# Optimization experiments

Hardware: AMD Instinct MI355X
Metric: run time of the kernel (lower is better)

## Reference

```python
import jax, jax.numpy as jnp
import numpy as np

B, S, D, E, H, K = 2, 2048, 1024, 8, 4096, 2


def setup_inputs() -> dict:
    key = jax.random.key(0)
    ks = jax.random.split(key, 7)
    sd = 1.0 / np.sqrt(D)
    sh = 1.0 / np.sqrt(H)
    return {
        "x": jax.random.normal(ks[0], (B, S, D), dtype=jnp.float32),
        "router_w": jax.random.uniform(ks[1], (D, E), jnp.float32, -sd, sd),
        "router_b": jnp.zeros((E,), jnp.float32),
        "w1": jax.random.uniform(ks[2], (E, D, H), jnp.float32, -sd, sd),
        "b1": jnp.zeros((E, H), jnp.float32),
        "w2": jax.random.uniform(ks[3], (E, H, D), jnp.float32, -sh, sh),
        "b2": jnp.zeros((E, D), jnp.float32),
    }


def reference(x, router_w, router_b, w1, b1, w2, b2):
    # Router: softmax over experts, then top-k and renormalize
    router_logits = jnp.einsum("bsd,de->bse", x, router_w) + router_b
    router_probs = jax.nn.softmax(router_logits, axis=-1)
    top_k_probs, top_k_indices = jax.lax.top_k(router_probs, K)  # [B,S,K]
    top_k_probs = top_k_probs / jnp.sum(top_k_probs, axis=-1, keepdims=True)

    # Dense all-expert FFN (Block assumed: Linear -> GELU -> Linear)
    h = jax.nn.gelu(jnp.einsum("bsd,edh->bseh", x, w1) + b1)  # [B,S,E,H]
    expert_outputs = jnp.einsum("bseh,ehd->bsed", h, w2) + b2  # [B,S,E,D]

    # Gather top-k experts per token and combine with renormalized probs
    idx = top_k_indices[..., None]  # [B,S,K,1]
    selected = jnp.take_along_axis(expert_outputs, idx, axis=2)  # [B,S,K,D]
    return jnp.sum(selected * top_k_probs[..., None], axis=2)  # [B,S,D]
```

## Files before the change

### kernel.cpp

```cpp
#include <hip/hip_runtime.h>
#include <hip/hip_bf16.h>

#define TOK   4096
#define DDIM  1024
#define NEXP  8
#define HDIM  4096
#define KSEL  2
#define NPAIR (TOK * KSEL)
#define NSPLIT 4

typedef __attribute__((ext_vector_type(8))) _Float16 f16x8;
typedef __attribute__((ext_vector_type(4))) _Float16 f16x4;
typedef __attribute__((ext_vector_type(4))) float    f32x4;

__device__ __forceinline__ void gload16(const void* g, void* l) {
  __builtin_amdgcn_global_load_lds((const __attribute__((address_space(1))) void*)g,
                                   (__attribute__((address_space(3))) void*)l, 16, 0, 0);
}

__device__ __forceinline__ float gelu_tanh(float u) {
  float inner = 0.7978845608028654f * (u + 0.044715f * u * u * u);
  float t2 = __expf(2.f * inner);
  return u - u / (t2 + 1.f);
}

__global__ __launch_bounds__(256) void k_router(const float* __restrict__ x,
    const float* __restrict__ rw, const float* __restrict__ rb,
    int* __restrict__ tidx, float* __restrict__ tw,
    _Float16* __restrict__ xb) {
  const int t    = blockIdx.x * 4 + (threadIdx.x >> 6);
  const int lane = threadIdx.x & 63;
  const float* xr = x + (size_t)t * DDIM;
  _Float16*   xbr = xb + (size_t)t * DDIM;
  float acc[NEXP];
#pragma unroll
  for (int e = 0; e < NEXP; ++e) acc[e] = 0.f;
  for (int d0 = lane * 4; d0 < DDIM; d0 += 256) {
    const float4 xv = *(const float4*)(xr + d0);
    f16x4 hx;
    hx[0] = (_Float16)xv.x; hx[1] = (_Float16)xv.y;
    hx[2] = (_Float16)xv.z; hx[3] = (_Float16)xv.w;
    *(f16x4*)(xbr + d0) = hx;
#pragma unroll
    for (int i = 0; i < 4; ++i) {
      const float xs = (&xv.x)[i];
      const float4 r0 = *(const float4*)(rw + (size_t)(d0 + i) * NEXP);
      const float4 r1 = *(const float4*)(rw + (size_t)(d0 + i) * NEXP + 4);
      acc[0] += xs * r0.x; acc[1] += xs * r0.y; acc[2] += xs * r0.z; acc[3] += xs * r0.w;
      acc[4] += xs * r1.x; acc[5] += xs * r1.y; acc[6] += xs * r1.z; acc[7] += xs * r1.w;
    }
  }
#pragma unroll
  for (int e = 0; e < NEXP; ++e) {
    float v = acc[e];
#pragma unroll
    for (int s = 32; s; s >>= 1) v += __shfl_xor(v, s, 64);
    acc[e] = v;
  }
  if (lane == 0) {
    float lg[NEXP];
#pragma unroll
    for (int e = 0; e < NEXP; ++e) lg[e] = acc[e] + rb[e];
    int i0 = 0;
#pragma unroll
    for (int e = 1; e < NEXP; ++e) if (lg[e] > lg[i0]) i0 = e;
    int i1 = -1; float best = -3.4e38f;
#pragma unroll
    for (int e = 0; e < NEXP; ++e) {
      if (e == i0) continue;
      if (lg[e] > best) { best = lg[e]; i1 = e; }
    }
    float w0 = 1.f / (1.f + expf(lg[i1] - lg[i0]));
    tidx[t * 2]     = i0;  tidx[t * 2 + 1] = i1;
    tw[t * 2]       = w0;  tw[t * 2 + 1]   = 1.f - w0;
  }
}

__global__ __launch_bounds__(1024) void k_scan(const int* __restrict__ tidx,
                       const float* __restrict__ tw,
                       int* __restrict__ offs,
                       int* __restrict__ row_token, float* __restrict__ row_w,
                       int* __restrict__ inv) {
  __shared__ int hist[NEXP];
  __shared__ int soff[NEXP + 1];
  __shared__ int scur[NEXP];
  if (threadIdx.x < NEXP) hist[threadIdx.x] = 0;
  __syncthreads();
  const int lane = threadIdx.x & 63;
  int e_loc[NPAIR / 1024];
#pragma unroll
  for (int it = 0; it < NPAIR / 1024; ++it) {
    const int p = it * 1024 + threadIdx.x;
    const int e = tidx[p];
    e_loc[it] = e;
#pragma unroll
    for (int ee = 0; ee < NEXP; ++ee) {
      unsigned long long m = __ballot(e == ee);
      if (m && lane == 0) atomicAdd(&hist[ee], __popcll(m));
    }
  }
  __syncthreads();
  if (threadIdx.x == 0) {
    int run = 0;
    for (int e = 0; e < NEXP; ++e) { soff[e] = run; scur[e] = run; run += hist[e]; }
    soff[NEXP] = run;
    for (int e = 0; e <= NEXP; ++e) offs[e] = soff[e];
  }
  __syncthreads();
#pragma unroll
  for (int it = 0; it < NPAIR / 1024; ++it) {
    const int p = it * 1024 + threadIdx.x;
    const int e = e_loc[it];
    int pos = 0;
#pragma unroll
    for (int ee = 0; ee < NEXP; ++ee) {
      unsigned long long m = __ballot(e == ee);
      if (!m) continue;
      int base = 0;
      if (lane == 0) base = atomicAdd(&scur[ee], __popcll(m));
      base = __shfl(base, 0, 64);
      if (e == ee) pos = base + __popcll(m & ((1ull << lane) - 1ull));
    }
    row_token[pos] = p >> 1;
    row_w[pos]     = tw[p];
    inv[p]         = pos;
  }
}

__global__ __launch_bounds__(256) void k_transpose2(const float* __restrict__ w1,
    const float* __restrict__ w2, _Float16* __restrict__ w1t, _Float16* __restrict__ w2t) {
  __shared__ _Float16 tile[64][72];
  const int zz = blockIdx.y;
  const float* ip; _Float16* op; int Rr, Cc, i0, j0;
  if (zz < NEXP) {
    ip = w1 + (size_t)zz * DDIM * HDIM;  op = w1t + (size_t)zz * DDIM * HDIM;
    Rr = DDIM; Cc = HDIM;
    i0 = (blockIdx.x >> 6) * 64; j0 = (blockIdx.x & 63) * 64;
  } else {
    ip = w2 + (size_t)(zz - NEXP) * HDIM * DDIM;  op = w2t + (size_t)(zz - NEXP) * HDIM * DDIM;
    Rr = HDIM; Cc = DDIM;
    i0 = (blockIdx.x >> 4) * 64; j0 = (blockIdx.x & 15) * 64;
  }
  const int tx = threadIdx.x & 15, ty = threadIdx.x >> 4;
#pragma unroll
  for (int rr = 0; rr < 4; ++rr) {
    int r = ty + rr * 16;
    float4 v = *(const float4*)(ip + (size_t)(i0 + r) * Cc + j0 + tx * 4);
    tile[r][tx * 4 + 0] = (_Float16)v.x;
    tile[r][tx * 4 + 1] = (_Float16)v.y;
    tile[r][tx * 4 + 2] = (_Float16)v.z;
    tile[r][tx * 4 + 3] = (_Float16)v.w;
  }
  __syncthreads();
#pragma unroll
  for (int cc = 0; cc < 4; ++cc) {
    int c = ty + cc * 16;
    f16x4 o;
#pragma unroll
    for (int k = 0; k < 4; ++k) o[k] = tile[tx * 4 + k][c];
    *(f16x4*)(op + (size_t)(j0 + c) * Rr + i0 + tx * 4) = o;
  }
}

#define BM 128
#define BN 128
#define BKK 32


__global__ __launch_bounds__(256) void k_gemm1(
    const _Float16* __restrict__ xb,
    const _Float16* __restrict__ w1t,
    const float* __restrict__ b1,
    const int* __restrict__ offs,
    const int* __restrict__ row_token,
    _Float16* __restrict__ hbuf) {
  const int e    = blockIdx.z;
  const int off0 = offs[e];
  const int ne   = offs[e + 1] - off0;
  const int m0   = blockIdx.y * BM;
  if (m0 >= ne) return;
  const int n0   = blockIdx.x * BN;
  const int mrem = ne - m0;

  __shared__ __align__(16) char smem[32768];

  const int tid = threadIdx.x;
  const int wv = tid >> 6, lane = tid & 63;
  const int l15 = lane & 15;
  const int wr = wv >> 1, wc = wv & 1;

  const int rA0 = (wv * 2 + 0) * 16 + (lane >> 2);
  const int rA1 = (wv * 2 + 1) * 16 + (lane >> 2);
  const char* a_c = (const char*)xb;
  const char* b_c = (const char*)(w1t + (size_t)e * HDIM * DDIM);
  const int rc0 = (rA0 < mrem) ? rA0 : (mrem - 1);
  const int rc1 = (rA1 < mrem) ? rA1 : (mrem - 1);
  const char* ap0 = a_c + (size_t)row_token[off0 + m0 + rc0] * (DDIM * 2)
                        + (((lane & 3) ^ ((rA0 >> 1) & 3)) << 4);
  const char* ap1 = a_c + (size_t)row_token[off0 + m0 + rc1] * (DDIM * 2)
                        + (((lane & 3) ^ ((rA1 >> 1) & 3)) << 4);
  const char* bp0 = b_c + (size_t)(n0 + rA0) * (DDIM * 2)
                        + (((lane & 3) ^ ((rA0 >> 1) & 3)) << 4);
  const char* bp1 = b_c + (size_t)(n0 + rA1) * (DDIM * 2)
                        + (((lane & 3) ^ ((rA1 >> 1) & 3)) << 4);
  char* ldsA0 = smem + (wv * 2 + 0) * 1024;
  char* ldsA1 = smem + (wv * 2 + 1) * 1024;
  char* ldsB0 = smem + 16384 + (wv * 2 + 0) * 1024;
  char* ldsB1 = smem + 16384 + (wv * 2 + 1) * 1024;

  const unsigned foff = (unsigned)(((lane >> 4) ^ ((l15 >> 1) & 3)) << 4);

  f32x4 acc[4][4] = {};
  const int NT = DDIM / BKK;

  gload16(ap0, ldsA0); gload16(ap1, ldsA1);
  gload16(bp0, ldsB0); gload16(bp1, ldsB1);
  asm volatile("s_waitcnt vmcnt(0)" ::: "memory");
  __builtin_amdgcn_s_barrier();

#pragma unroll 2
  for (int ks = 0; ks < NT; ++ks) {
    const int cur = ks & 1;
    if (ks + 1 < NT) {
      const int nb = (cur ^ 1) * 8192;
      const size_t kb = (size_t)(ks + 1) * 64;
      gload16(ap0 + kb, ldsA0 + nb); gload16(ap1 + kb, ldsA1 + nb);
      gload16(bp0 + kb, ldsB0 + nb); gload16(bp1 + kb, ldsB1 + nb);
    }
    const char* Ab = smem + cur * 8192;
    const char* Bb = smem + 16384 + cur * 8192;
    f16x8 af[4], bfr[4];
#pragma unroll
    for (int m = 0; m < 4; ++m)
      af[m] = *(const f16x8*)(Ab + (wr * 64 + m * 16 + l15) * 64 + foff);
#pragma unroll
    for (int n = 0; n < 4; ++n)
      bfr[n] = *(const f16x8*)(Bb + (wc * 64 + n * 16 + l15) * 64 + foff);
#pragma unroll
    for (int m = 0; m < 4; ++m)
#pragma unroll
      for (int n = 0; n < 4; ++n)
        acc[m][n] = __builtin_amdgcn_mfma_f32_16x16x32_f16(af[m], bfr[n], acc[m][n], 0, 0, 0);
    __builtin_amdgcn_sched_barrier(0);
    asm volatile("s_waitcnt vmcnt(0)" ::: "memory");
    __builtin_amdgcn_s_barrier();
  }

  float bias[4];
#pragma unroll
  for (int n = 0; n < 4; ++n)
    bias[n] = b1[(size_t)e * HDIM + n0 + wc * 64 + n * 16 + l15];
#pragma unroll
  for (int m = 0; m < 4; ++m) {
#pragma unroll
    for (int j = 0; j < 4; ++j) {
      int row = wr * 64 + m * 16 + (lane >> 4) * 4 + j;
#pragma unroll
      for (int n = 0; n < 4; ++n) {
        int col = wc * 64 + n * 16 + l15;
        *(_Float16*)(smem + (row << 8) + (((col << 1) ^ ((row & 15) << 4)))) =
            (_Float16)gelu_tanh(acc[m][n][j] + bias[n]);
      }
    }
  }
  __syncthreads();
  {
    const int srow = tid >> 1, half = tid & 1;
    if (srow < mrem) {
      _Float16* hr = hbuf + (size_t)(off0 + m0 + srow) * HDIM + n0 + half * 64;
#pragma unroll
      for (int i = 0; i < 8; ++i) {
        f16x8 v = *(const f16x8*)(smem + (srow << 8) + (((half * 128 + i * 16) ^ ((srow & 15) << 4))));
        *(f16x8*)(hr + i * 8) = v;
      }
    }
  }
}

template <bool YB>
__global__ __launch_bounds__(256) void k_gemm2(
    const _Float16* __restrict__ hbuf,
    const _Float16* __restrict__ w2t,
    const float* __restrict__ b2,
    const int* __restrict__ offs,
    const int* __restrict__ row_token,
    const float* __restrict__ row_w,
    _Float16* __restrict__ yb,
    float* __restrict__ out) {
  const int zz = blockIdx.z;
  const int e  = zz >> 2;
  const int kh = zz & 3;
  const int off0 = offs[e];
  const int ne   = offs[e + 1] - off0;
  const int m0   = blockIdx.y * BM;
  if (m0 >= ne) return;
  const int n0   = blockIdx.x * BN;
  const int mrem = ne - m0;

  __shared__ __align__(16) char smem[32768];

  const int tid = threadIdx.x;
  const int wv = tid >> 6, lane = tid & 63;
  const int l15 = lane & 15;
  const int wr = wv >> 1, wc = wv & 1;

  const int rA0 = (wv * 2 + 0) * 16 + (lane >> 2);
  const int rA1 = (wv * 2 + 1) * 16 + (lane >> 2);
  const char* a_c = (const char*)hbuf;
  const char* b_c = (const char*)(w2t + (size_t)e * DDIM * HDIM);
  const int rc0 = (rA0 < mrem) ? rA0 : (mrem - 1);
  const int rc1 = (rA1 < mrem) ? rA1 : (mrem - 1);
  const size_t khb = (size_t)kh * ((HDIM / NSPLIT) * 2);
  const char* ap0 = a_c + (size_t)(off0 + m0 + rc0) * (HDIM * 2) + khb
                        + (((lane & 3) ^ ((rA0 >> 1) & 3)) << 4);
  const char* ap1 = a_c + (size_t)(off0 + m0 + rc1) * (HDIM * 2) + khb
                        + (((lane & 3) ^ ((rA1 >> 1) & 3)) << 4);
  const char* bp0 = b_c + (size_t)(n0 + rA0) * (HDIM * 2) + khb
                        + (((lane & 3) ^ ((rA0 >> 1) & 3)) << 4);
  const char* bp1 = b_c + (size_t)(n0 + rA1) * (HDIM * 2) + khb
                        + (((lane & 3) ^ ((rA1 >> 1) & 3)) << 4);
  char* ldsA0 = smem + (wv * 2 + 0) * 1024;
  char* ldsA1 = smem + (wv * 2 + 1) * 1024;
  char* ldsB0 = smem + 16384 + (wv * 2 + 0) * 1024;
  char* ldsB1 = smem + 16384 + (wv * 2 + 1) * 1024;

  const unsigned foff = (unsigned)(((lane >> 4) ^ ((l15 >> 1) & 3)) << 4);

  f32x4 acc[4][4] = {};
  const int NT = (HDIM / NSPLIT) / BKK;

  gload16(ap0, ldsA0); gload16(ap1, ldsA1);
  gload16(bp0, ldsB0); gload16(bp1, ldsB1);
  asm volatile("s_waitcnt vmcnt(0)" ::: "memory");
  __builtin_amdgcn_s_barrier();

#pragma unroll 2
  for (int ks = 0; ks < NT; ++ks) {
    const int cur = ks & 1;
    if (ks + 1 < NT) {
      const int nb = (cur ^ 1) * 8192;
      const size_t kb = (size_t)(ks + 1) * 64;
      gload16(ap0 + kb, ldsA0 + nb); gload16(ap1 + kb, ldsA1 + nb);
      gload16(bp0 + kb, ldsB0 + nb); gload16(bp1 + kb, ldsB1 + nb);
    }
    const char* Ab = smem + cur * 8192;
    const char* Bb = smem + 16384 + cur * 8192;
    f16x8 af[4], bfr[4];
#pragma unroll
    for (int m = 0; m < 4; ++m)
      af[m] = *(const f16x8*)(Ab + (wr * 64 + m * 16 + l15) * 64 + foff);
#pragma unroll
    for (int n = 0; n < 4; ++n)
      bfr[n] = *(const f16x8*)(Bb + (wc * 64 + n * 16 + l15) * 64 + foff);
#pragma unroll
    for (int m = 0; m < 4; ++m)
#pragma unroll
      for (int n = 0; n < 4; ++n)
        acc[m][n] = __builtin_amdgcn_mfma_f32_16x16x32_f16(af[m], bfr[n], acc[m][n], 0, 0, 0);
    __builtin_amdgcn_sched_barrier(0);
    asm volatile("s_waitcnt vmcnt(0)" ::: "memory");
    __builtin_amdgcn_s_barrier();
  }

  if (YB) {
    _Float16* ypart = yb + (size_t)kh * NPAIR * DDIM;
#pragma unroll
    for (int m = 0; m < 4; ++m) {
#pragma unroll
      for (int j = 0; j < 4; ++j) {
        int row = wr * 64 + m * 16 + (lane >> 4) * 4 + j;
#pragma unroll
        for (int n = 0; n < 4; ++n) {
          int col = wc * 64 + n * 16 + l15;
          *(_Float16*)(smem + (row << 8) + (((col << 1) ^ ((row & 15) << 4)))) =
              (_Float16)acc[m][n][j];
        }
      }
    }
    __syncthreads();
    const int srow = tid >> 1, half = tid & 1;
    if (srow < mrem) {
      _Float16* yr = ypart + (size_t)(off0 + m0 + srow) * DDIM + n0 + half * 64;
#pragma unroll
      for (int i = 0; i < 8; ++i) {
        f16x8 v = *(const f16x8*)(smem + (srow << 8) + (((half * 128 + i * 16) ^ ((srow & 15) << 4))));
        *(f16x8*)(yr + i * 8) = v;
      }
    }
  } else {
    float bias[4];
#pragma unroll
    for (int n = 0; n < 4; ++n)
      bias[n] = (kh == 0) ? b2[(size_t)e * DDIM + n0 + wc * 64 + n * 16 + l15] : 0.f;
#pragma unroll
    for (int m = 0; m < 4; ++m) {
#pragma unroll
      for (int j = 0; j < 4; ++j) {
        int row = wr * 64 + m * 16 + (lane >> 4) * 4 + j;
        if (row < mrem) {
          int g = off0 + m0 + row;
          float wgt = row_w[g];
          float* op = out + (size_t)row_token[g] * DDIM + n0 + wc * 64 + l15;
#pragma unroll
          for (int n = 0; n < 4; ++n)
            atomicAdd(op + n * 16, wgt * (acc[m][n][j] + bias[n]));
        }
      }
    }
  }
}

__global__ __launch_bounds__(256) void k_combine(const _Float16* __restrict__ yb,
    const int* __restrict__ inv, const int* __restrict__ tidx,
    const float* __restrict__ tw, const float* __restrict__ b2,
    float* __restrict__ out) {
  const int t  = blockIdx.x * 2 + (threadIdx.x >> 7);
  const int c8 = (threadIdx.x & 127) * 8;
  const int g0 = inv[2 * t],  g1 = inv[2 * t + 1];
  const int e0 = tidx[2 * t], e1 = tidx[2 * t + 1];
  const float w0 = tw[2 * t], w1 = tw[2 * t + 1];
  float s0[8] = {0,0,0,0,0,0,0,0}, s1[8] = {0,0,0,0,0,0,0,0};
#pragma unroll
  for (int p = 0; p < NSPLIT; ++p) {
    const _Float16* yp = yb + (size_t)p * NPAIR * DDIM;
    f16x8 a = *(const f16x8*)(yp + (size_t)g0 * DDIM + c8);
    f16x8 b = *(const f16x8*)(yp + (size_t)g1 * DDIM + c8);
#pragma unroll
    for (int i = 0; i < 8; ++i) { s0[i] += (float)a[i]; s1[i] += (float)b[i]; }
  }
  float o[8];
#pragma unroll
  for (int i = 0; i < 8; ++i) {
    float bA = b2[(size_t)e0 * DDIM + c8 + i];
    float bB = b2[(size_t)e1 * DDIM + c8 + i];
    o[i] = w0 * (s0[i] + bA) + w1 * (s1[i] + bB);
  }
  float* op = out + (size_t)t * DDIM + c8;
  *(float4*)op       = make_float4(o[0], o[1], o[2], o[3]);
  *(float4*)(op + 4) = make_float4(o[4], o[5], o[6], o[7]);
}

extern "C" void kernel_launch(void* const* d_in, const int* in_sizes, int n_in,
                              void* d_out, int out_size, void* d_ws, size_t ws_size,
                              hipStream_t stream) {
  const float* x  = (const float*)d_in[0];
  const float* rw = (const float*)d_in[1];
  const float* rb = (const float*)d_in[2];
  const float* w1 = (const float*)d_in[3];
  const float* b1 = (const float*)d_in[4];
  const float* w2 = (const float*)d_in[5];
  const float* b2 = (const float*)d_in[6];
  float* out = (float*)d_out;
  char* ws = (char*)d_ws;

  int*      tidx    = (int*)(ws + 0);
  float*    tw      = (float*)(ws + 32768);
  int*      offs    = (int*)(ws + 65792);
  int*      row_tok = (int*)(ws + 66048);
  float*    row_w   = (float*)(ws + 98816);
  int*      inv     = (int*)(ws + 131584);
  _Float16* xb      = (_Float16*)(ws + 164352);
  _Float16* wtA     = (_Float16*)(ws + 8552960);
  _Float16* wtB     = (_Float16*)(ws + 75661824);
  _Float16* hb      = (_Float16*)(ws + 142770688);
  _Float16* yb      = wtA;
  const bool big = ws_size >= 209879552ULL;

  if (!big) hipMemsetAsync(out, 0, (size_t)TOK * DDIM * sizeof(float), stream);

  k_router<<<dim3(TOK / 4), 256, 0, stream>>>(x, rw, rb, tidx, tw, xb);
  k_scan<<<dim3(1), 1024, 0, stream>>>(tidx, tw, offs, row_tok, row_w, inv);
  k_transpose2<<<dim3(1024, 2 * NEXP), 256, 0, stream>>>(w1, w2, wtA, wtB);
  k_gemm1<<<dim3(HDIM / BN, TOK / BM, NEXP), 256, 0, stream>>>(xb, wtA, b1, offs, row_tok, hb);
  if (big) {
    k_gemm2<true><<<dim3(DDIM / BN, TOK / BM, NEXP * NSPLIT), 256, 0, stream>>>(
        hb, wtB, b2, offs, row_tok, row_w, yb, out);
    k_combine<<<dim3(TOK / 2), 256, 0, stream>>>(yb, inv, tidx, tw, b2, out);
  } else {
    k_gemm2<false><<<dim3(DDIM / BN, TOK / BM, NEXP * NSPLIT), 256, 0, stream>>>(
        hb, wtB, b2, offs, row_tok, row_w, yb, out);
  }
}
```

Measured before the change: 385.5 us.

## Use compact tile list for grouped GEMMs and overlap prefetch with barrier

The scan kernel now builds a compact list of (expert, m-tile) pairs, and both grouped GEMMs launch a flat 1D grid over that list instead of a sparse 3D grid where most blocks exit early. The K-loop now waits with vmcnt(4) so the next tile's loads stay in flight while the current one is consumed, rather than fully draining every iteration. The atomic-output fallback path is removed, so the fp16 split-K buffer and combine kernel are always used. MAXT=72 caps the tile count, which assumes expert loads never need more than 72 tiles.

Measured after the change: 356.0 us. 7.7% less time.

```diff
diff --git a/kernel.cpp b/kernel.cpp
--- a/kernel.cpp
+++ b/kernel.cpp
@@ -8,6 +8,7 @@
 #define KSEL  2
 #define NPAIR (TOK * KSEL)
 #define NSPLIT 4
+#define MAXT  72
 
 typedef __attribute__((ext_vector_type(8))) _Float16 f16x8;
 typedef __attribute__((ext_vector_type(4))) _Float16 f16x4;
@@ -80,7 +81,8 @@
                        const float* __restrict__ tw,
                        int* __restrict__ offs,
                        int* __restrict__ row_token, float* __restrict__ row_w,
-                       int* __restrict__ inv) {
+                       int* __restrict__ inv,
+                       int* __restrict__ tlist, int* __restrict__ tcount) {
   __shared__ int hist[NEXP];
   __shared__ int soff[NEXP + 1];
   __shared__ int scur[NEXP];
@@ -105,6 +107,12 @@
     for (int e = 0; e < NEXP; ++e) { soff[e] = run; scur[e] = run; run += hist[e]; }
     soff[NEXP] = run;
     for (int e = 0; e <= NEXP; ++e) offs[e] = soff[e];
+    int cnt = 0;
+    for (int e = 0; e < NEXP; ++e) {
+      const int ne = soff[e + 1] - soff[e];
+      for (int m = 0; m < ne; m += 128) tlist[cnt++] = (e << 8) | (m >> 7);
+    }
+    *tcount = cnt;
   }
   __syncthreads();
 #pragma unroll
@@ -173,13 +181,17 @@
     const float* __restrict__ b1,
     const int* __restrict__ offs,
     const int* __restrict__ row_token,
+    const int* __restrict__ tlist, const int* __restrict__ tcount,
     _Float16* __restrict__ hbuf) {
-  const int e    = blockIdx.z;
+  const int bid = blockIdx.x;
+  const int t   = bid >> 5;
+  if (t >= *tcount) return;
+  const int tl  = tlist[t];
+  const int e   = tl >> 8;
+  const int m0  = (tl & 255) * BM;
+  const int n0  = (bid & 31) * BN;
   const int off0 = offs[e];
   const int ne   = offs[e + 1] - off0;
-  const int m0   = blockIdx.y * BM;
-  if (m0 >= ne) return;
-  const int n0   = blockIdx.x * BN;
   const int mrem = ne - m0;
 
   __shared__ __align__(16) char smem[32768];
@@ -215,8 +227,6 @@
 
   gload16(ap0, ldsA0); gload16(ap1, ldsA1);
   gload16(bp0, ldsB0); gload16(bp1, ldsB1);
-  asm volatile("s_waitcnt vmcnt(0)" ::: "memory");
-  __builtin_amdgcn_s_barrier();
 
 #pragma unroll 2
   for (int ks = 0; ks < NT; ++ks) {
@@ -226,7 +236,12 @@
       const size_t kb = (size_t)(ks + 1) * 64;
       gload16(ap0 + kb, ldsA0 + nb); gload16(ap1 + kb, ldsA1 + nb);
       gload16(bp0 + kb, ldsB0 + nb); gload16(bp1 + kb, ldsB1 + nb);
-    }
+      asm volatile("s_waitcnt vmcnt(4)" ::: "memory");
+    } else {
+      asm volatile("s_waitcnt vmcnt(0)" ::: "memory");
+    }
+    __builtin_amdgcn_sched_barrier(0);
+    __builtin_amdgcn_s_barrier();
     const char* Ab = smem + cur * 8192;
     const char* Bb = smem + 16384 + cur * 8192;
     f16x8 af[4], bfr[4];
@@ -242,7 +257,6 @@
       for (int n = 0; n < 4; ++n)
         acc[m][n] = __builtin_amdgcn_mfma_f32_16x16x32_f16(af[m], bfr[n], acc[m][n], 0, 0, 0);
     __builtin_amdgcn_sched_barrier(0);
-    asm volatile("s_waitcnt vmcnt(0)" ::: "memory");
     __builtin_amdgcn_s_barrier();
   }
 
@@ -277,24 +291,23 @@
   }
 }
 
-template <bool YB>
 __global__ __launch_bounds__(256) void k_gemm2(
     const _Float16* __restrict__ hbuf,
     const _Float16* __restrict__ w2t,
-    const float* __restrict__ b2,
     const int* __restrict__ offs,
-    const int* __restrict__ row_token,
-    const float* __restrict__ row_w,
-    _Float16* __restrict__ yb,
-    float* __restrict__ out) {
-  const int zz = blockIdx.z;
-  const int e  = zz >> 2;
-  const int kh = zz & 3;
+    const int* __restrict__ tlist, const int* __restrict__ tcount,
+    _Float16* __restrict__ yb) {
+  const int bid = blockIdx.x;
+  const int t   = bid >> 5;
+  if (t >= *tcount) return;
+  const int tl  = tlist[t];
+  const int e   = tl >> 8;
+  const int m0  = (tl & 255) * BM;
+  const int sub = bid & 31;
+  const int kh  = sub >> 3;
+  const int n0  = (sub & 7) * BN;
   const int off0 = offs[e];
   const int ne   = offs[e + 1] - off0;
-  const int m0   = blockIdx.y * BM;
-  if (m0 >= ne) return;
-  const int n0   = blockIdx.x * BN;
   const int mrem = ne - m0;
 
   __shared__ __align__(16) char smem[32768];
@@ -331,8 +344,6 @@
 
   gload16(ap0, ldsA0); gload16(ap1, ldsA1);
   gload16(bp0, ldsB0); gload16(bp1, ldsB1);
-  asm volatile("s_waitcnt vmcnt(0)" ::: "memory");
-  __builtin_amdgcn_s_barrier();
 
 #pragma unroll 2
   for (int ks = 0; ks < NT; ++ks) {
@@ -342,7 +353,12 @@
       const size_t kb = (size_t)(ks + 1) * 64;
       gload16(ap0 + kb, ldsA0 + nb); gload16(ap1 + kb, ldsA1 + nb);
       gload16(bp0 + kb, ldsB0 + nb); gload16(bp1 + kb, ldsB1 + nb);
-    }
+      asm volatile("s_waitcnt vmcnt(4)" ::: "memory");
+    } else {
+      asm volatile("s_waitcnt vmcnt(0)" ::: "memory");
+    }
+    __builtin_amdgcn_sched_barrier(0);
+    __builtin_amdgcn_s_barrier();
     const char* Ab = smem + cur * 8192;
     const char* Bb = smem + 16384 + cur * 8192;
     f16x8 af[4], bfr[4];
@@ -358,26 +374,25 @@
       for (int n = 0; n < 4; ++n)
         acc[m][n] = __builtin_amdgcn_mfma_f32_16x16x32_f16(af[m], bfr[n], acc[m][n], 0, 0, 0);
     __builtin_amdgcn_sched_barrier(0);
-    asm volatile("s_waitcnt vmcnt(0)" ::: "memory");
     __builtin_amdgcn_s_barrier();
   }
 
-  if (YB) {
-    _Float16* ypart = yb + (size_t)kh * NPAIR * DDIM;
-#pragma unroll
-    for (int m = 0; m < 4; ++m) {
-#pragma unroll
-      for (int j = 0; j < 4; ++j) {
-        int row = wr * 64 + m * 16 + (lane >> 4) * 4 + j;
-#pragma unroll
-        for (int n = 0; n < 4; ++n) {
-          int col = wc * 64 + n * 16 + l15;
-          *(_Float16*)(smem + (row << 8) + (((col << 1) ^ ((row & 15) << 4)))) =
-              (_Float16)acc[m][n][j];
-        }
+  _Float16* ypart = yb + (size_t)kh * NPAIR * DDIM;
+#pragma unroll
+  for (int m = 0; m < 4; ++m) {
+#pragma unroll
+    for (int j = 0; j < 4; ++j) {
+      int row = wr * 64 + m * 16 + (lane >> 4) * 4 + j;
+#pragma unroll
+      for (int n = 0; n < 4; ++n) {
+        int col = wc * 64 + n * 16 + l15;
+        *(_Float16*)(smem + (row << 8) + (((col << 1) ^ ((row & 15) << 4)))) =
+            (_Float16)acc[m][n][j];
       }
     }
-    __syncthreads();
+  }
+  __syncthreads();
+  {
     const int srow = tid >> 1, half = tid & 1;
     if (srow < mrem) {
       _Float16* yr = ypart + (size_t)(off0 + m0 + srow) * DDIM + n0 + half * 64;
@@ -385,26 +400,6 @@
       for (int i = 0; i < 8; ++i) {
         f16x8 v = *(const f16x8*)(smem + (srow << 8) + (((half * 128 + i * 16) ^ ((srow & 15) << 4))));
         *(f16x8*)(yr + i * 8) = v;
-      }
-    }
-  } else {
-    float bias[4];
-#pragma unroll
-    for (int n = 0; n < 4; ++n)
-      bias[n] = (kh == 0) ? b2[(size_t)e * DDIM + n0 + wc * 64 + n * 16 + l15] : 0.f;
-#pragma unroll
-    for (int m = 0; m < 4; ++m) {
-#pragma unroll
-      for (int j = 0; j < 4; ++j) {
-        int row = wr * 64 + m * 16 + (lane >> 4) * 4 + j;
-        if (row < mrem) {
-          int g = off0 + m0 + row;
-          float wgt = row_w[g];
-          float* op = out + (size_t)row_token[g] * DDIM + n0 + wc * 64 + l15;
-#pragma unroll
-          for (int n = 0; n < 4; ++n)
-            atomicAdd(op + n * 16, wgt * (acc[m][n][j] + bias[n]));
-        }
       }
     }
   }
@@ -455,7 +450,9 @@
 
   int*      tidx    = (int*)(ws + 0);
   float*    tw      = (float*)(ws + 32768);
-  int*      offs    = (int*)(ws + 65792);
+  int*      tcount  = (int*)(ws + 65536);
+  int*      tlist   = (int*)(ws + 65544);
+  int*      offs    = (int*)(ws + 65856);
   int*      row_tok = (int*)(ws + 66048);
   float*    row_w   = (float*)(ws + 98816);
   int*      inv     = (int*)(ws + 131584);
@@ -464,20 +461,11 @@
   _Float16* wtB     = (_Float16*)(ws + 75661824);
   _Float16* hb      = (_Float16*)(ws + 142770688);
   _Float16* yb      = wtA;
-  const bool big = ws_size >= 209879552ULL;
-
-  if (!big) hipMemsetAsync(out, 0, (size_t)TOK * DDIM * sizeof(float), stream);
 
   k_router<<<dim3(TOK / 4), 256, 0, stream>>>(x, rw, rb, tidx, tw, xb);
-  k_scan<<<dim3(1), 1024, 0, stream>>>(tidx, tw, offs, row_tok, row_w, inv);
+  k_scan<<<dim3(1), 1024, 0, stream>>>(tidx, tw, offs, row_tok, row_w, inv, tlist, tcount);
   k_transpose2<<<dim3(1024, 2 * NEXP), 256, 0, stream>>>(w1, w2, wtA, wtB);
-  k_gemm1<<<dim3(HDIM / BN, TOK / BM, NEXP), 256, 0, stream>>>(xb, wtA, b1, offs, row_tok, hb);
-  if (big) {
-    k_gemm2<true><<<dim3(DDIM / BN, TOK / BM, NEXP * NSPLIT), 256, 0, stream>>>(
-        hb, wtB, b2, offs, row_tok, row_w, yb, out);
-    k_combine<<<dim3(TOK / 2), 256, 0, stream>>>(yb, inv, tidx, tw, b2, out);
-  } else {
-    k_gemm2<false><<<dim3(DDIM / BN, TOK / BM, NEXP * NSPLIT), 256, 0, stream>>>(
-        hb, wtB, b2, offs, row_tok, row_w, yb, out);
-  }
-}
+  k_gemm1<<<dim3(MAXT * 32), 256, 0, stream>>>(xb, wtA, b1, offs, row_tok, tlist, tcount, hb);
+  k_gemm2<<<dim3(MAXT * 32), 256, 0, stream>>>(hb, wtB, offs, tlist, tcount, yb);
+  k_combine<<<dim3(TOK / 2), 256, 0, stream>>>(yb, inv, tidx, tw, b2, out);
+}
```
